# Kernel optimization log

Hardware: AMD Instinct MI355X
Metric: run time of the kernel (lower is better)

Reference implementation:

```python
import jax, jax.numpy as jnp
import numpy as np

NUM_EMBEDDINGS = 1024
EMBEDDING_DIM = 128
COMMITMENT_COST = 0.25
B, T = 32, 2048


def setup_inputs() -> dict:
    key = jax.random.key(0)
    k1, k2 = jax.random.split(key)
    inputs = jax.random.normal(k1, (B, T, EMBEDDING_DIM), dtype=jnp.float32)
    lim = 1.0 / NUM_EMBEDDINGS
    embedding_weight = jax.random.uniform(
        k2, (NUM_EMBEDDINGS, EMBEDDING_DIM), dtype=jnp.float32,
        minval=-lim, maxval=lim)
    return {"inputs": inputs, "embedding_weight": embedding_weight}


def reference(inputs, embedding_weight):
    D = embedding_weight.shape[1]
    flat = inputs.reshape(-1, D)                                  # [N, D]
    # squared L2 distances to every codebook entry: [N, K]
    distances = (
        jnp.sum(flat * flat, axis=1, keepdims=True)
        + jnp.sum(embedding_weight * embedding_weight, axis=1)
        - 2.0 * jnp.matmul(flat, embedding_weight.T)
    )
    encoding_indices = jnp.argmin(distances, axis=1)              # [N]
    quantized = embedding_weight[encoding_indices].reshape(inputs.shape)
    sg = jax.lax.stop_gradient
    e_latent_loss = jnp.mean((sg(quantized) - inputs) ** 2)
    q_latent_loss = jnp.mean((quantized - sg(inputs)) ** 2)
    loss = q_latent_loss + COMMITMENT_COST * e_latent_loss
    # straight-through estimator
    quantized = inputs + sg(quantized - inputs)
    return (loss, quantized, encoding_indices)
```

## Files before the change

kernel.cpp:

```cpp
#include <hip/hip_runtime.h>

#define NROWS 65536
#define KC    1024
#define DIM   128
#define W_DIST 5e-5f

typedef short  bf16x8 __attribute__((ext_vector_type(8)));
typedef float  f32x4  __attribute__((ext_vector_type(4)));
typedef float  f32x16 __attribute__((ext_vector_type(16)));

#define ZERO16 ((f32x16){0.f,0.f,0.f,0.f,0.f,0.f,0.f,0.f,0.f,0.f,0.f,0.f,0.f,0.f,0.f,0.f})

__device__ __forceinline__ unsigned short f2bf_rne(float f) {
    unsigned int u = __float_as_uint(f);
    u += 0x7FFFu + ((u >> 16) & 1u);
    return (unsigned short)(u >> 16);
}
__device__ __forceinline__ float bf2f(unsigned short h) {
    return __uint_as_float(((unsigned int)h) << 16);
}

__device__ __forceinline__ void gll16(const unsigned short* g, short* l) {
    __builtin_amdgcn_global_load_lds(
        (const __attribute__((address_space(1))) unsigned int*)g,
        (__attribute__((address_space(3))) unsigned int*)l,
        16, 0, 0);
}

template <int N>
__device__ __forceinline__ void vmwait() {
    if constexpr (N == 8)      asm volatile("s_waitcnt vmcnt(8)" ::: "memory");
    else if constexpr (N == 4) asm volatile("s_waitcnt vmcnt(4)" ::: "memory");
    else if constexpr (N == 2) asm volatile("s_waitcnt vmcnt(2)" ::: "memory");
    else                       asm volatile("s_waitcnt vmcnt(0)" ::: "memory");
}

__device__ __forceinline__ float np_sumsq_128(const float* v) {
    float r[8];
    #pragma unroll
    for (int j = 0; j < 8; ++j) r[j] = __fmul_rn(v[j], v[j]);
    #pragma unroll
    for (int i = 1; i < 16; ++i)
        #pragma unroll
        for (int j = 0; j < 8; ++j)
            r[j] = __fadd_rn(r[j], __fmul_rn(v[i * 8 + j], v[i * 8 + j]));
    return __fadd_rn(__fadd_rn(__fadd_rn(r[0], r[1]), __fadd_rn(r[2], r[3])),
                     __fadd_rn(__fadd_rn(r[4], r[5]), __fadd_rn(r[6], r[7])));
}

__global__ __launch_bounds__(256) void vq_prep(const float* __restrict__ emb,
        float* __restrict__ enorm,
        unsigned short* __restrict__ eh, unsigned short* __restrict__ em) {
    const int k = blockIdx.x * 256 + threadIdx.x;
    if (k >= KC) return;
    float v[DIM];
    const float4* e = reinterpret_cast<const float4*>(emb + (size_t)k * DIM);
    #pragma unroll
    for (int i = 0; i < 32; ++i) {
        float4 t = e[i];
        v[i * 4 + 0] = t.x; v[i * 4 + 1] = t.y;
        v[i * 4 + 2] = t.z; v[i * 4 + 3] = t.w;
    }
    enorm[k] = np_sumsq_128(v);
    unsigned short* ph = eh + (size_t)k * DIM;
    unsigned short* pm = em + (size_t)k * DIM;
    #pragma unroll
    for (int i = 0; i < 16; ++i) {
        unsigned int h[8], m[8];
        #pragma unroll
        for (int j = 0; j < 8; ++j) {
            float f = v[i * 8 + j];
            unsigned short hh = f2bf_rne(f);
            h[j] = hh;
            m[j] = f2bf_rne(f - bf2f(hh));
        }
        uint4 vh = {h[0] | (h[1] << 16), h[2] | (h[3] << 16),
                    h[4] | (h[5] << 16), h[6] | (h[7] << 16)};
        uint4 vm = {m[0] | (m[1] << 16), m[2] | (m[3] << 16),
                    m[4] | (m[5] << 16), m[6] | (m[7] << 16)};
        *reinterpret_cast<uint4*>(ph + i * 8) = vh;
        *reinterpret_cast<uint4*>(pm + i * 8) = vm;
    }
}

__global__ __launch_bounds__(256, 2) void vq_mfma(
        const float* __restrict__ x,
        const unsigned short* __restrict__ eh, const unsigned short* __restrict__ em,
        const float* __restrict__ enorm,
        int* __restrict__ bestk, float* __restrict__ idx_out,
        int* __restrict__ fb_cnt, int* __restrict__ fb_rows) {
    const int tid  = threadIdx.x;
    const int lane = tid & 63;
    const int wid  = tid >> 6;
    const int lr31 = lane & 31;
    const int hi   = lane >> 5;
    const int rtile = blockIdx.x * 128 + wid * 32;

    __shared__ short ldsE[3][2][4096];
    __shared__ float s_enorm[KC];

    const int u0 = wid * 128 + lane;
    const int u1 = wid * 128 + 64 + lane;
    const int src0 = (u0 & 31) * DIM + (u0 >> 5) * 8;
    const int src1 = (u1 & 31) * DIM + (u1 >> 5) * 8;
    const int dst0 = wid * 128 * 8;
    const int dst1 = (wid * 128 + 64) * 8;

#define VQ_STAGE(T, B)                                                      \
    do {                                                                    \
        const unsigned short* _gh = eh + (size_t)(T) * 4096;                \
        const unsigned short* _gm = em + (size_t)(T) * 4096;                \
        gll16(_gh + src0, &ldsE[B][0][dst0]);                               \
        gll16(_gh + src1, &ldsE[B][0][dst1]);                               \
        gll16(_gm + src0, &ldsE[B][1][dst0]);                               \
        gll16(_gm + src1, &ldsE[B][1][dst1]);                               \
    } while (0)

    bf16x8 fxh[8], fxm[8];
    {
        const float* px = x + (size_t)(rtile + lr31) * DIM + hi * 8;
        #pragma unroll
        for (int s = 0; s < 8; ++s) {
            float4 a = *reinterpret_cast<const float4*>(px + s * 16);
            float4 b = *reinterpret_cast<const float4*>(px + s * 16 + 4);
            float f[8] = {a.x, a.y, a.z, a.w, b.x, b.y, b.z, b.w};
            bf16x8 vh, vm;
            #pragma unroll
            for (int j = 0; j < 8; ++j) {
                unsigned short hh = f2bf_rne(f[j]);
                vh[j] = (short)hh;
                vm[j] = (short)f2bf_rne(f[j] - bf2f(hh));
            }
            fxh[s] = vh; fxm[s] = vm;
        }
    }
    #pragma unroll
    for (int s = 0; s < 8; ++s)
        asm volatile("" : "+v"(fxh[s]), "+v"(fxm[s]));

    *reinterpret_cast<float4*>(&s_enorm[tid * 4]) =
        *reinterpret_cast<const float4*>(&enorm[tid * 4]);

    VQ_STAGE(0, 0);
    VQ_STAGE(1, 1);

    asm volatile("s_waitcnt lgkmcnt(0)" ::: "memory");
    __builtin_amdgcn_s_barrier();

    float m1 = 1e30f, m2 = 1e30f; int k1 = 0;
    f32x16 aE, dE, aO, dO;

#define VQ_EPI(T, PA, PD)                                                   \
    do {                                                                    \
        const int _kb = (T) * 32 + (hi << 2);                               \
        _Pragma("unroll")                                                   \
        for (int g = 0; g < 4; ++g) {                                       \
            const f32x4 _nr = *reinterpret_cast<const f32x4*>(&s_enorm[_kb + g * 8]); \
            _Pragma("unroll")                                               \
            for (int j = 0; j < 4; ++j) {                                   \
                const int _r = g * 4 + j;                                   \
                float _v = fmaf(-2.0f, PA[_r] + PD[_r], _nr[j]);            \
                int _kk = _kb + g * 8 + j;                                  \
                bool _lt = _v < m1;                                         \
                m2 = fminf(m2, fmaxf(m1, _v));                              \
                k1 = _lt ? _kk : k1;                                        \
                m1 = fminf(m1, _v);                                         \
            }                                                               \
        }                                                                   \
    } while (0)

#define VQ_ITER(T, B, SB, CA, CD, PA, PD, VMN, DOSTAGE, DOEPI)              \
    do {                                                                    \
        vmwait<VMN>();                                                      \
        __builtin_amdgcn_s_barrier();                                       \
        asm volatile("" ::: "memory");                                      \
        CA = ZERO16; CD = ZERO16;                                           \
        __builtin_amdgcn_s_setprio(1);                                      \
        _Pragma("unroll")                                                   \
        for (int s = 0; s < 8; ++s) {                                       \
            const int _u = ((s * 2 + hi) * 32 + lr31) * 8;                  \
            bf16x8 feh = *reinterpret_cast<const bf16x8*>(&ldsE[B][0][_u]); \
            bf16x8 fem = *reinterpret_cast<const bf16x8*>(&ldsE[B][1][_u]); \
            CA = __builtin_amdgcn_mfma_f32_32x32x16_bf16(feh, fxh[s], CA, 0, 0, 0); \
            CD = __builtin_amdgcn_mfma_f32_32x32x16_bf16(feh, fxm[s], CD, 0, 0, 0); \
            CD = __builtin_amdgcn_mfma_f32_32x32x16_bf16(fem, fxh[s], CD, 0, 0, 0); \
        }                                                                   \
        __builtin_amdgcn_s_setprio(0);                                      \
        if (DOSTAGE) { VQ_STAGE((T) + 2, SB); }                             \
        if (DOEPI)   { VQ_EPI((T) - 1, PA, PD); }                           \
    } while (0)

    VQ_ITER(0, 0, 2, aE, dE, aO, dO, 4, 1, 0);
    VQ_ITER(1, 1, 0, aO, dO, aE, dE, 4, 1, 1);
    VQ_ITER(2, 2, 1, aE, dE, aO, dO, 4, 1, 1);
    VQ_ITER(3, 0, 2, aO, dO, aE, dE, 4, 1, 1);
    VQ_ITER(4, 1, 0, aE, dE, aO, dO, 4, 1, 1);
    VQ_ITER(5, 2, 1, aO, dO, aE, dE, 4, 1, 1);
    for (int tb = 6; tb < 30; tb += 6) {
        VQ_ITER(tb + 0, 0, 2, aE, dE, aO, dO, 4, 1, 1);
        VQ_ITER(tb + 1, 1, 0, aO, dO, aE, dE, 4, 1, 1);
        VQ_ITER(tb + 2, 2, 1, aE, dE, aO, dO, 4, 1, 1);
        VQ_ITER(tb + 3, 0, 2, aO, dO, aE, dE, 4, 1, 1);
        VQ_ITER(tb + 4, 1, 0, aE, dE, aO, dO, 4, 1, 1);
        VQ_ITER(tb + 5, 2, 1, aO, dO, aE, dE, 4, 1, 1);
    }
    VQ_ITER(30, 0, 2, aE, dE, aO, dO, 4, 0, 1);
    VQ_ITER(31, 1, 0, aO, dO, aE, dE, 0, 0, 1);
    VQ_EPI(31, aO, dO);
#undef VQ_ITER
#undef VQ_EPI
#undef VQ_STAGE

    {
        float om1 = __shfl_xor(m1, 32, 64);
        float om2 = __shfl_xor(m2, 32, 64);
        int   ok1 = __shfl_xor(k1, 32, 64);
        float mx = fmaxf(m1, om1);
        m2 = fminf(fminf(m2, om2), mx);
        bool take = (om1 < m1) || (om1 == m1 && ok1 < k1);
        k1 = take ? ok1 : k1;
        m1 = fminf(m1, om1);
    }
    if (lane < 32) {
        const int row = rtile + lane;
        if (m2 - m1 < W_DIST) {
            int slot = atomicAdd(fb_cnt, 1);
            fb_rows[slot] = row;
        } else {
            bestk[row] = k1;
            idx_out[row] = (float)k1;
        }
    }
}

__global__ __launch_bounds__(512) void vq_fallback(
        const float* __restrict__ x, const float* __restrict__ emb,
        const float* __restrict__ enorm,
        const int* __restrict__ fb_cnt, const int* __restrict__ fb_rows,
        int* __restrict__ bestk, float* __restrict__ idx_out) {
    const int tid  = threadIdx.x;
    const int lane = tid & 63;
    const int wid  = tid >> 6;
    const int nb = *fb_cnt;

    __shared__ float sx[8][DIM];
    __shared__ float s_xn[8];
    __shared__ float swv[8][8];
    __shared__ int   swk[8][8];

    const float en0 = enorm[tid];
    const float en1 = enorm[tid + 512];
    const float4* e0p = reinterpret_cast<const float4*>(emb + (size_t)tid * DIM);
    const float4* e1p = reinterpret_cast<const float4*>(emb + (size_t)(tid + 512) * DIM);

    for (int base = blockIdx.x * 8; base < nb; base += gridDim.x * 8) {
        const int R = min(8, nb - base);
        {
            const int r = tid >> 6;
            const int c2 = (tid & 63) * 2;
            const int slot = fb_rows[min(base + r, nb - 1)];
            float2 v = *reinterpret_cast<const float2*>(x + (size_t)slot * DIM + c2);
            sx[r][c2] = v.x; sx[r][c2 + 1] = v.y;
        }
        __syncthreads();
        if (tid < 8) s_xn[tid] = np_sumsq_128(&sx[tid][0]);
        __syncthreads();

        float a0[8][4], a1[8][4];
        #pragma unroll
        for (int r = 0; r < 8; ++r)
            #pragma unroll
            for (int c = 0; c < 4; ++c) { a0[r][c] = 0.f; a1[r][c] = 0.f; }

        for (int q = 0; q < 32; ++q) {
            float4 ev0 = e0p[q];
            float4 ev1 = e1p[q];
            #pragma unroll
            for (int r = 0; r < 8; ++r) {
                float4 xv = *reinterpret_cast<const float4*>(&sx[r][q * 4]);
                a0[r][0] = fmaf(xv.x, ev0.x, a0[r][0]);
                a0[r][1] = fmaf(xv.y, ev0.y, a0[r][1]);
                a0[r][2] = fmaf(xv.z, ev0.z, a0[r][2]);
                a0[r][3] = fmaf(xv.w, ev0.w, a0[r][3]);
                a1[r][0] = fmaf(xv.x, ev1.x, a1[r][0]);
                a1[r][1] = fmaf(xv.y, ev1.y, a1[r][1]);
                a1[r][2] = fmaf(xv.z, ev1.z, a1[r][2]);
                a1[r][3] = fmaf(xv.w, ev1.w, a1[r][3]);
            }
        }

        float cv[8]; int ck[8];
        #pragma unroll
        for (int r = 0; r < 8; ++r) {
            float xn = s_xn[r];
            float d0 = __fadd_rn(__fadd_rn(a0[r][0], a0[r][1]),
                                 __fadd_rn(a0[r][2], a0[r][3]));
            float s0 = __fsub_rn(__fadd_rn(xn, en0), __fmul_rn(2.0f, d0));
            float d1 = __fadd_rn(__fadd_rn(a1[r][0], a1[r][1]),
                                 __fadd_rn(a1[r][2], a1[r][3]));
            float s1 = __fsub_rn(__fadd_rn(xn, en1), __fmul_rn(2.0f, d1));
            bool t1 = (s1 < s0);
            cv[r] = t1 ? s1 : s0;
            ck[r] = t1 ? tid + 512 : tid;
        }
        #pragma unroll
        for (int off = 1; off < 64; off <<= 1) {
            #pragma unroll
            for (int r = 0; r < 8; ++r) {
                float ov = __shfl_xor(cv[r], off, 64);
                int   ok = __shfl_xor(ck[r], off, 64);
                bool take = (ov < cv[r]) || (ov == cv[r] && ok < ck[r]);
                cv[r] = take ? ov : cv[r];
                ck[r] = take ? ok : ck[r];
            }
        }
        if (lane == 0) {
            #pragma unroll
            for (int r = 0; r < 8; ++r) { swv[wid][r] = cv[r]; swk[wid][r] = ck[r]; }
        }
        __syncthreads();
        if (tid < R) {
            float bv = swv[0][tid]; int bk = swk[0][tid];
            #pragma unroll
            for (int w = 1; w < 8; ++w) {
                float v = swv[w][tid]; int k = swk[w][tid];
                bool take = (v < bv) || (v == bv && k < bk);
                bv = take ? v : bv;
                bk = take ? k : bk;
            }
            const int row = fb_rows[base + tid];
            bestk[row] = bk;
            idx_out[row] = (float)bk;
        }
        __syncthreads();
    }
}

__global__ __launch_bounds__(256) void vq_gather(
        const float* __restrict__ x, const float* __restrict__ emb,
        const int* __restrict__ bestk, float* __restrict__ quant,
        double* __restrict__ partials) {
    const int t = blockIdx.x * 256 + threadIdx.x;
    const int r = t >> 4;
    const int c = (t & 15) * 8;
    const int bk = bestk[r];
    const float4* ep = reinterpret_cast<const float4*>(emb + (size_t)bk * DIM + c);
    const float4* xp = reinterpret_cast<const float4*>(x + (size_t)r * DIM + c);
    float4 e0 = ep[0], e1 = ep[1];
    float4 x0 = xp[0], x1 = xp[1];
    float* q = quant + (size_t)r * DIM + c;
    q[0] = e0.x; q[1] = e0.y; q[2] = e0.z; q[3] = e0.w;
    q[4] = e1.x; q[5] = e1.y; q[6] = e1.z; q[7] = e1.w;
    float d0 = e0.x - x0.x, d1 = e0.y - x0.y, d2 = e0.z - x0.z, d3 = e0.w - x0.w;
    float d4 = e1.x - x1.x, d5 = e1.y - x1.y, d6 = e1.z - x1.z, d7 = e1.w - x1.w;
    float acc = fmaf(d0, d0, fmaf(d1, d1, fmaf(d2, d2, d3 * d3)))
              + fmaf(d4, d4, fmaf(d5, d5, fmaf(d6, d6, d7 * d7)));
    #pragma unroll
    for (int off = 32; off > 0; off >>= 1) acc += __shfl_down(acc, off, 64);

    __shared__ float sacc[4];
    if ((threadIdx.x & 63) == 0) sacc[threadIdx.x >> 6] = acc;
    __syncthreads();
    if (threadIdx.x == 0)
        partials[blockIdx.x] =
            (double)sacc[0] + (double)sacc[1] + (double)sacc[2] + (double)sacc[3];
}

__global__ __launch_bounds__(256) void vq_loss(
        const double* __restrict__ partials, float* __restrict__ out) {
    double s = 0.0;
    #pragma unroll
    for (int i = 0; i < 16; ++i) s += partials[threadIdx.x + i * 256];
    #pragma unroll
    for (int off = 32; off > 0; off >>= 1) s += __shfl_down(s, off, 64);
    __shared__ double sd[4];
    if ((threadIdx.x & 63) == 0) sd[threadIdx.x >> 6] = s;
    __syncthreads();
    if (threadIdx.x == 0)
        out[0] = (float)((sd[0] + sd[1] + sd[2] + sd[3]) * (1.25 / 8388608.0));
}

extern "C" void kernel_launch(void* const* d_in, const int* in_sizes, int n_in,
                              void* d_out, int out_size, void* d_ws, size_t ws_size,
                              hipStream_t stream) {
    const float* x   = (const float*)d_in[0];
    const float* emb = (const float*)d_in[1];

    float* out      = (float*)d_out;
    float* loss_out = out;
    float* quant    = out + 1;
    float* idx_out  = out + 1 + (size_t)NROWS * DIM;

    char* ws = (char*)d_ws;
    int*    fb_cnt   = (int*)(ws + 8);
    float*  enorm    = (float*)(ws + 1024);
    int*    fb_rows  = (int*)(ws + 16384);
    int*    bestk    = (int*)(ws + 278528);
    unsigned short* eh = (unsigned short*)(ws + 557056);
    unsigned short* em = (unsigned short*)(ws + 819200);
    double* partials = (double*)(ws + 1081344);

    hipMemsetAsync(ws, 0, 16, stream);
    vq_prep<<<4, 256, 0, stream>>>(emb, enorm, eh, em);
    vq_mfma<<<512, 256, 0, stream>>>(x, eh, em, enorm,
                                     bestk, idx_out, fb_cnt, fb_rows);
    vq_fallback<<<1024, 512, 0, stream>>>(x, emb, enorm, fb_cnt, fb_rows,
                                          bestk, idx_out);
    vq_gather<<<4096, 256, 0, stream>>>(x, emb, bestk, quant, partials);
    vq_loss<<<1, 256, 0, stream>>>(partials, loss_out);
}
```

Measured before the change: 110.4 us.

## Restructure codebook pipeline to double-buffered 64-entry stages with split MFMA accumulators

Replaces the triple-buffered 32-codeword software pipeline with a double-buffered loop over 64-codeword stages. Half the waves load hi parts and half load mid parts. Each stage issues the next prefetch right after the barrier and keeps three independent accumulators per 32-entry half, so fewer MFMAs form a dependent chain. The epilogue now runs right after its own MFMAs instead of overlapping the next tile, and there are half as many barriers. The fallback scalar loop is also batched to load four embedding vectors at a time. The costs are a full vmcnt(0) wait per stage, more accumulator registers, and the loss of epilogue/MFMA interleaving.

Result: slower. 117.4 us (+6.4%).

```diff
diff --git a/kernel.cpp b/kernel.cpp
--- a/kernel.cpp
+++ b/kernel.cpp
@@ -25,14 +25,6 @@
         (const __attribute__((address_space(1))) unsigned int*)g,
         (__attribute__((address_space(3))) unsigned int*)l,
         16, 0, 0);
-}
-
-template <int N>
-__device__ __forceinline__ void vmwait() {
-    if constexpr (N == 8)      asm volatile("s_waitcnt vmcnt(8)" ::: "memory");
-    else if constexpr (N == 4) asm volatile("s_waitcnt vmcnt(4)" ::: "memory");
-    else if constexpr (N == 2) asm volatile("s_waitcnt vmcnt(2)" ::: "memory");
-    else                       asm volatile("s_waitcnt vmcnt(0)" ::: "memory");
 }
 
 __device__ __forceinline__ float np_sumsq_128(const float* v) {
@@ -96,25 +88,27 @@
     const int hi   = lane >> 5;
     const int rtile = blockIdx.x * 128 + wid * 32;
 
-    __shared__ short ldsE[3][2][4096];
+    __shared__ short bufE[2][2][8192];
     __shared__ float s_enorm[KC];
 
-    const int u0 = wid * 128 + lane;
-    const int u1 = wid * 128 + 64 + lane;
-    const int src0 = (u0 & 31) * DIM + (u0 >> 5) * 8;
-    const int src1 = (u1 & 31) * DIM + (u1 >> 5) * 8;
-    const int dst0 = wid * 128 * 8;
-    const int dst1 = (wid * 128 + 64) * 8;
-
-#define VQ_STAGE(T, B)                                                      \
+    const unsigned short* gpart = (wid < 2) ? eh : em;
+    int loff[8];
+    #pragma unroll
+    for (int i = 0; i < 8; ++i) {
+        const int u = ((wid & 1) * 512 + i * 64 + lane) & 1023;
+        loff[i] = ((u >> 9) * 32 + (u & 31)) * DIM + ((u >> 5) & 15) * 8;
+    }
+
+#define VQ_STAGE(SP, DB)                                                    \
     do {                                                                    \
-        const unsigned short* _gh = eh + (size_t)(T) * 4096;                \
-        const unsigned short* _gm = em + (size_t)(T) * 4096;                \
-        gll16(_gh + src0, &ldsE[B][0][dst0]);                               \
-        gll16(_gh + src1, &ldsE[B][0][dst1]);                               \
-        gll16(_gm + src0, &ldsE[B][1][dst0]);                               \
-        gll16(_gm + src1, &ldsE[B][1][dst1]);                               \
+        const unsigned short* _g = gpart + (size_t)(SP) * 8192;             \
+        _Pragma("unroll")                                                   \
+        for (int i = 0; i < 8; ++i)                                         \
+            gll16(_g + loff[i],                                             \
+                  &bufE[DB][wid >> 1][((wid & 1) * 512 + i * 64) * 8]);     \
     } while (0)
+
+    VQ_STAGE(0, 0);
 
     bf16x8 fxh[8], fxm[8];
     {
@@ -140,17 +134,11 @@
 
     *reinterpret_cast<float4*>(&s_enorm[tid * 4]) =
         *reinterpret_cast<const float4*>(&enorm[tid * 4]);
-
-    VQ_STAGE(0, 0);
-    VQ_STAGE(1, 1);
-
     asm volatile("s_waitcnt lgkmcnt(0)" ::: "memory");
-    __builtin_amdgcn_s_barrier();
 
     float m1 = 1e30f, m2 = 1e30f; int k1 = 0;
-    f32x16 aE, dE, aO, dO;
-
-#define VQ_EPI(T, PA, PD)                                                   \
+
+#define VQ_EPI(T, PA, PB, PC)                                               \
     do {                                                                    \
         const int _kb = (T) * 32 + (hi << 2);                               \
         _Pragma("unroll")                                                   \
@@ -159,7 +147,7 @@
             _Pragma("unroll")                                               \
             for (int j = 0; j < 4; ++j) {                                   \
                 const int _r = g * 4 + j;                                   \
-                float _v = fmaf(-2.0f, PA[_r] + PD[_r], _nr[j]);            \
+                float _v = fmaf(-2.0f, (PA[_r] + PB[_r]) + PC[_r], _nr[j]); \
                 int _kk = _kb + g * 8 + j;                                  \
                 bool _lt = _v < m1;                                         \
                 m2 = fminf(m2, fmaxf(m1, _v));                              \
@@ -169,45 +157,37 @@
         }                                                                   \
     } while (0)
 
-#define VQ_ITER(T, B, SB, CA, CD, PA, PD, VMN, DOSTAGE, DOEPI)              \
-    do {                                                                    \
-        vmwait<VMN>();                                                      \
-        __builtin_amdgcn_s_barrier();                                       \
-        asm volatile("" ::: "memory");                                      \
-        CA = ZERO16; CD = ZERO16;                                           \
-        __builtin_amdgcn_s_setprio(1);                                      \
-        _Pragma("unroll")                                                   \
-        for (int s = 0; s < 8; ++s) {                                       \
-            const int _u = ((s * 2 + hi) * 32 + lr31) * 8;                  \
-            bf16x8 feh = *reinterpret_cast<const bf16x8*>(&ldsE[B][0][_u]); \
-            bf16x8 fem = *reinterpret_cast<const bf16x8*>(&ldsE[B][1][_u]); \
-            CA = __builtin_amdgcn_mfma_f32_32x32x16_bf16(feh, fxh[s], CA, 0, 0, 0); \
-            CD = __builtin_amdgcn_mfma_f32_32x32x16_bf16(feh, fxm[s], CD, 0, 0, 0); \
-            CD = __builtin_amdgcn_mfma_f32_32x32x16_bf16(fem, fxh[s], CD, 0, 0, 0); \
-        }                                                                   \
-        __builtin_amdgcn_s_setprio(0);                                      \
-        if (DOSTAGE) { VQ_STAGE((T) + 2, SB); }                             \
-        if (DOEPI)   { VQ_EPI((T) - 1, PA, PD); }                           \
-    } while (0)
-
-    VQ_ITER(0, 0, 2, aE, dE, aO, dO, 4, 1, 0);
-    VQ_ITER(1, 1, 0, aO, dO, aE, dE, 4, 1, 1);
-    VQ_ITER(2, 2, 1, aE, dE, aO, dO, 4, 1, 1);
-    VQ_ITER(3, 0, 2, aO, dO, aE, dE, 4, 1, 1);
-    VQ_ITER(4, 1, 0, aE, dE, aO, dO, 4, 1, 1);
-    VQ_ITER(5, 2, 1, aO, dO, aE, dE, 4, 1, 1);
-    for (int tb = 6; tb < 30; tb += 6) {
-        VQ_ITER(tb + 0, 0, 2, aE, dE, aO, dO, 4, 1, 1);
-        VQ_ITER(tb + 1, 1, 0, aO, dO, aE, dE, 4, 1, 1);
-        VQ_ITER(tb + 2, 2, 1, aE, dE, aO, dO, 4, 1, 1);
-        VQ_ITER(tb + 3, 0, 2, aO, dO, aE, dE, 4, 1, 1);
-        VQ_ITER(tb + 4, 1, 0, aE, dE, aO, dO, 4, 1, 1);
-        VQ_ITER(tb + 5, 2, 1, aO, dO, aE, dE, 4, 1, 1);
-    }
-    VQ_ITER(30, 0, 2, aE, dE, aO, dO, 4, 0, 1);
-    VQ_ITER(31, 1, 0, aO, dO, aE, dE, 0, 0, 1);
-    VQ_EPI(31, aO, dO);
-#undef VQ_ITER
+    for (int S = 0; S < 16; ++S) {
+        asm volatile("s_waitcnt vmcnt(0)" ::: "memory");
+        __builtin_amdgcn_s_barrier();
+        asm volatile("" ::: "memory");
+        if (S < 15) VQ_STAGE(S + 1, (S + 1) & 1);
+        const int db = S & 1;
+        f32x16 A0 = ZERO16, B0 = ZERO16, C0 = ZERO16;
+        f32x16 A1 = ZERO16, B1 = ZERO16, C1 = ZERO16;
+        __builtin_amdgcn_s_setprio(1);
+        #pragma unroll
+        for (int s = 0; s < 8; ++s) {
+            const int o = ((s * 2 + hi) * 32 + lr31) * 8;
+            bf16x8 feh = *reinterpret_cast<const bf16x8*>(&bufE[db][0][o]);
+            bf16x8 fem = *reinterpret_cast<const bf16x8*>(&bufE[db][1][o]);
+            A0 = __builtin_amdgcn_mfma_f32_32x32x16_bf16(feh, fxh[s], A0, 0, 0, 0);
+            B0 = __builtin_amdgcn_mfma_f32_32x32x16_bf16(feh, fxm[s], B0, 0, 0, 0);
+            C0 = __builtin_amdgcn_mfma_f32_32x32x16_bf16(fem, fxh[s], C0, 0, 0, 0);
+        }
+        #pragma unroll
+        for (int s = 0; s < 8; ++s) {
+            const int o = 4096 + ((s * 2 + hi) * 32 + lr31) * 8;
+            bf16x8 feh = *reinterpret_cast<const bf16x8*>(&bufE[db][0][o]);
+            bf16x8 fem = *reinterpret_cast<const bf16x8*>(&bufE[db][1][o]);
+            A1 = __builtin_amdgcn_mfma_f32_32x32x16_bf16(feh, fxh[s], A1, 0, 0, 0);
+            B1 = __builtin_amdgcn_mfma_f32_32x32x16_bf16(feh, fxm[s], B1, 0, 0, 0);
+            C1 = __builtin_amdgcn_mfma_f32_32x32x16_bf16(fem, fxh[s], C1, 0, 0, 0);
+        }
+        __builtin_amdgcn_s_setprio(0);
+        VQ_EPI(2 * S,     A0, B0, C0);
+        VQ_EPI(2 * S + 1, A1, B1, C1);
+    }
 #undef VQ_EPI
 #undef VQ_STAGE
 
@@ -272,20 +252,24 @@
             #pragma unroll
             for (int c = 0; c < 4; ++c) { a0[r][c] = 0.f; a1[r][c] = 0.f; }
 
-        for (int q = 0; q < 32; ++q) {
-            float4 ev0 = e0p[q];
-            float4 ev1 = e1p[q];
-            #pragma unroll
-            for (int r = 0; r < 8; ++r) {
-                float4 xv = *reinterpret_cast<const float4*>(&sx[r][q * 4]);
-                a0[r][0] = fmaf(xv.x, ev0.x, a0[r][0]);
-                a0[r][1] = fmaf(xv.y, ev0.y, a0[r][1]);
-                a0[r][2] = fmaf(xv.z, ev0.z, a0[r][2]);
-                a0[r][3] = fmaf(xv.w, ev0.w, a0[r][3]);
-                a1[r][0] = fmaf(xv.x, ev1.x, a1[r][0]);
-                a1[r][1] = fmaf(xv.y, ev1.y, a1[r][1]);
-                a1[r][2] = fmaf(xv.z, ev1.z, a1[r][2]);
-                a1[r][3] = fmaf(xv.w, ev1.w, a1[r][3]);
+        for (int q = 0; q < 32; q += 4) {
+            float4 e0v[4], e1v[4];
+            #pragma unroll
+            for (int j = 0; j < 4; ++j) { e0v[j] = e0p[q + j]; e1v[j] = e1p[q + j]; }
+            #pragma unroll
+            for (int j = 0; j < 4; ++j) {
+                #pragma unroll
+                for (int r = 0; r < 8; ++r) {
+                    float4 xv = *reinterpret_cast<const float4*>(&sx[r][(q + j) * 4]);
+                    a0[r][0] = fmaf(xv.x, e0v[j].x, a0[r][0]);
+                    a0[r][1] = fmaf(xv.y, e0v[j].y, a0[r][1]);
+                    a0[r][2] = fmaf(xv.z, e0v[j].z, a0[r][2]);
+                    a0[r][3] = fmaf(xv.w, e0v[j].w, a0[r][3]);
+                    a1[r][0] = fmaf(xv.x, e1v[j].x, a1[r][0]);
+                    a1[r][1] = fmaf(xv.y, e1v[j].y, a1[r][1]);
+                    a1[r][2] = fmaf(xv.z, e1v[j].z, a1[r][2]);
+                    a1[r][3] = fmaf(xv.w, e1v[j].w, a1[r][3]);
+                }
             }
         }
 
```

## Restructure fallback argmin to stage codebook tiles in padded shared memory

Applied to the files above, without the earlier changes.

The fp32 fallback kernel for near-tie rows is rewritten so that each block stages 64-entry codebook tiles into padded LDS, cooperatively loaded with coalesced float4 reads. Each thread then computes one (row, codeword) dot product per tile, replacing the old scheme where each thread streamed two full codebook rows from global memory and kept 64 accumulators. The aim is to cut register pressure and uncoalesced global traffic. In exchange it adds 16 extra barrier pairs per row group and a sequential running-min per thread. The tie-breaking order is kept.

Measured after the change: 117.4 us. 6.3% more time.

```diff
diff --git a/kernel.cpp b/kernel.cpp
--- a/kernel.cpp
+++ b/kernel.cpp
@@ -4,6 +4,7 @@
 #define KC    1024
 #define DIM   128
 #define W_DIST 5e-5f
+#define FB_PAD 132
 
 typedef short  bf16x8 __attribute__((ext_vector_type(8)));
 typedef float  f32x4  __attribute__((ext_vector_type(4)));
@@ -241,96 +242,79 @@
     const int tid  = threadIdx.x;
     const int lane = tid & 63;
     const int wid  = tid >> 6;
+    const int r    = tid & 7;
+    const int kg   = tid >> 3;
     const int nb = *fb_cnt;
 
-    __shared__ float sx[8][DIM];
+    __shared__ float sx[8][FB_PAD];
+    __shared__ float sE[64][FB_PAD];
     __shared__ float s_xn[8];
     __shared__ float swv[8][8];
     __shared__ int   swk[8][8];
 
-    const float en0 = enorm[tid];
-    const float en1 = enorm[tid + 512];
-    const float4* e0p = reinterpret_cast<const float4*>(emb + (size_t)tid * DIM);
-    const float4* e1p = reinterpret_cast<const float4*>(emb + (size_t)(tid + 512) * DIM);
-
     for (int base = blockIdx.x * 8; base < nb; base += gridDim.x * 8) {
         const int R = min(8, nb - base);
         {
-            const int r = tid >> 6;
+            const int rr = tid >> 6;
             const int c2 = (tid & 63) * 2;
-            const int slot = fb_rows[min(base + r, nb - 1)];
+            const int slot = fb_rows[min(base + rr, nb - 1)];
             float2 v = *reinterpret_cast<const float2*>(x + (size_t)slot * DIM + c2);
-            sx[r][c2] = v.x; sx[r][c2 + 1] = v.y;
+            sx[rr][c2] = v.x; sx[rr][c2 + 1] = v.y;
         }
         __syncthreads();
         if (tid < 8) s_xn[tid] = np_sumsq_128(&sx[tid][0]);
-        __syncthreads();
-
-        float a0[8][4], a1[8][4];
+
+        float bv = 3.402823466e38f; int bk = 0;
+        for (int kt = 0; kt < 16; ++kt) {
+            __syncthreads();
+            {
+                const float4* g = reinterpret_cast<const float4*>(
+                    emb + (size_t)kt * 64 * DIM);
+                #pragma unroll
+                for (int i = 0; i < 4; ++i) {
+                    const int u = tid * 4 + i;
+                    float4 v = g[u];
+                    *reinterpret_cast<float4*>(&sE[u >> 5][(u & 31) * 4]) = v;
+                }
+            }
+            __syncthreads();
+            const int k = kt * 64 + kg;
+            float d0 = 0.f, d1 = 0.f, d2 = 0.f, d3 = 0.f;
+            #pragma unroll
+            for (int q = 0; q < 32; ++q) {
+                float4 ev = *reinterpret_cast<const float4*>(&sE[kg][q * 4]);
+                float4 xv = *reinterpret_cast<const float4*>(&sx[r][q * 4]);
+                d0 = fmaf(xv.x, ev.x, d0);
+                d1 = fmaf(xv.y, ev.y, d1);
+                d2 = fmaf(xv.z, ev.z, d2);
+                d3 = fmaf(xv.w, ev.w, d3);
+            }
+            float dot = __fadd_rn(__fadd_rn(d0, d1), __fadd_rn(d2, d3));
+            float s = __fsub_rn(__fadd_rn(s_xn[r], enorm[k]), __fmul_rn(2.0f, dot));
+            if (s < bv) { bv = s; bk = k; }
+        }
         #pragma unroll
-        for (int r = 0; r < 8; ++r)
-            #pragma unroll
-            for (int c = 0; c < 4; ++c) { a0[r][c] = 0.f; a1[r][c] = 0.f; }
-
-        for (int q = 0; q < 32; ++q) {
-            float4 ev0 = e0p[q];
-            float4 ev1 = e1p[q];
-            #pragma unroll
-            for (int r = 0; r < 8; ++r) {
-                float4 xv = *reinterpret_cast<const float4*>(&sx[r][q * 4]);
-                a0[r][0] = fmaf(xv.x, ev0.x, a0[r][0]);
-                a0[r][1] = fmaf(xv.y, ev0.y, a0[r][1]);
-                a0[r][2] = fmaf(xv.z, ev0.z, a0[r][2]);
-                a0[r][3] = fmaf(xv.w, ev0.w, a0[r][3]);
-                a1[r][0] = fmaf(xv.x, ev1.x, a1[r][0]);
-                a1[r][1] = fmaf(xv.y, ev1.y, a1[r][1]);
-                a1[r][2] = fmaf(xv.z, ev1.z, a1[r][2]);
-                a1[r][3] = fmaf(xv.w, ev1.w, a1[r][3]);
-            }
-        }
-
-        float cv[8]; int ck[8];
-        #pragma unroll
-        for (int r = 0; r < 8; ++r) {
-            float xn = s_xn[r];
-            float d0 = __fadd_rn(__fadd_rn(a0[r][0], a0[r][1]),
-                                 __fadd_rn(a0[r][2], a0[r][3]));
-            float s0 = __fsub_rn(__fadd_rn(xn, en0), __fmul_rn(2.0f, d0));
-            float d1 = __fadd_rn(__fadd_rn(a1[r][0], a1[r][1]),
-                                 __fadd_rn(a1[r][2], a1[r][3]));
-            float s1 = __fsub_rn(__fadd_rn(xn, en1), __fmul_rn(2.0f, d1));
-            bool t1 = (s1 < s0);
-            cv[r] = t1 ? s1 : s0;
-            ck[r] = t1 ? tid + 512 : tid;
-        }
-        #pragma unroll
-        for (int off = 1; off < 64; off <<= 1) {
-            #pragma unroll
-            for (int r = 0; r < 8; ++r) {
-                float ov = __shfl_xor(cv[r], off, 64);
-                int   ok = __shfl_xor(ck[r], off, 64);
-                bool take = (ov < cv[r]) || (ov == cv[r] && ok < ck[r]);
-                cv[r] = take ? ov : cv[r];
-                ck[r] = take ? ok : ck[r];
-            }
-        }
-        if (lane == 0) {
-            #pragma unroll
-            for (int r = 0; r < 8; ++r) { swv[wid][r] = cv[r]; swk[wid][r] = ck[r]; }
-        }
+        for (int off = 8; off <= 32; off <<= 1) {
+            float ov = __shfl_xor(bv, off, 64);
+            int   ok = __shfl_xor(bk, off, 64);
+            bool take = (ov < bv) || (ov == bv && ok < bk);
+            bv = take ? ov : bv;
+            bk = take ? ok : bk;
+        }
+        if (lane < 8) { swv[wid][lane] = bv; swk[wid][lane] = bk; }
         __syncthreads();
         if (tid < R) {
-            float bv = swv[0][tid]; int bk = swk[0][tid];
+            float fv = swv[0][tid]; int fk = swk[0][tid];
             #pragma unroll
             for (int w = 1; w < 8; ++w) {
-                float v = swv[w][tid]; int k = swk[w][tid];
-                bool take = (v < bv) || (v == bv && k < bk);
-                bv = take ? v : bv;
-                bk = take ? k : bk;
+                float v = swv[w][tid]; int k2 = swk[w][tid];
+                bool take = (v < fv) || (v == fv && k2 < fk);
+                fv = take ? v : fv;
+                fk = take ? k2 : fk;
             }
             const int row = fb_rows[base + tid];
-            bestk[row] = bk;
-            idx_out[row] = (float)bk;
+            bestk[row] = fk;
+            idx_out[row] = (float)fk;
         }
         __syncthreads();
     }
```
